# Kernel optimization log

Measured on AMD Instinct MI355X. Metric: run time of the kernel, lower is better.

Reference implementation:

```python
import math
import jax, jax.numpy as jnp
import numpy as np

B, L, D = 8, 2048, 1024
NEG_INF = 1e9  # config.INF stand-in; large finite value keeps fully-masked rows NaN-free


def setup_inputs() -> dict:
    key = jax.random.key(0)
    k1, k2, k3, k4, k5, k6 = jax.random.split(key, 6)
    s = 1.0 / math.sqrt(D)
    return {
        "input_seq": jax.random.normal(k1, (B, L, D), dtype=jnp.float32),
        "input_lens": jax.random.randint(k2, (B,), 1, L + 1, dtype=jnp.int64),
        "output_seq": jax.random.normal(k3, (B, L, D), dtype=jnp.float32),
        "Wk": jax.random.normal(k4, (D, D), dtype=jnp.float32) * s,
        "Wv": jax.random.normal(k5, (D, D), dtype=jnp.float32) * s,
        "Wq": jax.random.normal(k6, (D, D), dtype=jnp.float32) * s,
    }


def reference(input_seq, input_lens, output_seq, Wk, Wv, Wq):
    # Linear(embed_dim, embed_dim, bias=False): y = x @ W^T
    k = jnp.einsum('bld,ed->ble', input_seq, Wk)   # [B, L, D]
    v = jnp.einsum('bld,ed->ble', input_seq, Wv)   # [B, L, D]
    q = jnp.einsum('bld,ed->ble', output_seq, Wq)  # [B, L, D]

    scores = jnp.einsum('bqd,bkd->bqk', q, k) / math.sqrt(D)  # [B, Lq, Lk]

    # Faithful to the torch code (apply_mask=True): mask [B, L] is unsqueezed
    # on the LAST dim -> [B, L, 1], so it broadcasts over the KEY axis and
    # effectively masks query rows with index >= input_lens.
    valid = jnp.arange(L)[None, :] < input_lens[:, None]      # [B, L]
    scores = jnp.where(valid[:, :, None], scores, -NEG_INF)

    attn = jax.nn.softmax(scores, axis=-1)                    # [B, Lq, Lk]
    # dropout is identity in eval mode (deterministic reference)
    context = jnp.einsum('bqk,bkd->bqd', attn, v)             # [B, Lq, D]
    return context, attn
```

## Files before the change

### kernel.cpp

```cpp
#include <hip/hip_runtime.h>
#include <hip/hip_bf16.h>

#define B_ 8
#define L_ 2048
#define D_ 1024
#define CTX_ELEMS (B_ * L_ * D_)

typedef __bf16 bf16x8 __attribute__((ext_vector_type(8)));
typedef float f32x4 __attribute__((ext_vector_type(4)));
typedef unsigned short u16x8 __attribute__((ext_vector_type(8)));
typedef unsigned short u16x4 __attribute__((ext_vector_type(4)));

typedef __attribute__((address_space(1))) void GV;
typedef __attribute__((address_space(3))) void LV;
#define GLL16(g, l) __builtin_amdgcn_global_load_lds((GV*)(g), (LV*)(l), 16, 0, 0)

__device__ __forceinline__ unsigned short f2bf(float f) {
    union { float f; unsigned u; } c; c.f = f;
    unsigned u = c.u;
    u += 0x7fffu + ((u >> 16) & 1u);
    return (unsigned short)(u >> 16);
}

__global__ __launch_bounds__(256) void cvt_kernel(
    const float* __restrict__ x, const float* __restrict__ y,
    const float* __restrict__ Wk, const float* __restrict__ Wv,
    const float* __restrict__ Wq,
    unsigned short* __restrict__ xb, unsigned short* __restrict__ yb,
    unsigned short* __restrict__ wkb, unsigned short* __restrict__ wvb,
    unsigned short* __restrict__ wqb)
{
    const float* src; unsigned short* dst; int n4;
    switch (blockIdx.y) {
        case 0:  src = x;  dst = xb;  n4 = CTX_ELEMS / 4; break;
        case 1:  src = y;  dst = yb;  n4 = CTX_ELEMS / 4; break;
        case 2:  src = Wk; dst = wkb; n4 = D_ * D_ / 4;   break;
        case 3:  src = Wv; dst = wvb; n4 = D_ * D_ / 4;   break;
        default: src = Wq; dst = wqb; n4 = D_ * D_ / 4;   break;
    }
    const int stride = gridDim.x * 256;
    for (int i = blockIdx.x * 256 + threadIdx.x; i < n4; i += stride) {
        float4 f = ((const float4*)src)[i];
        u16x4 o = { f2bf(f.x), f2bf(f.y), f2bf(f.z), f2bf(f.w) };
        ((u16x4*)dst)[i] = o;
    }
}

#define BARx()  __builtin_amdgcn_s_barrier()
#define LGKM0() do { asm volatile("s_waitcnt lgkmcnt(0)" ::: "memory"); \
                     __builtin_amdgcn_sched_barrier(0); } while (0)
#define PRIO(p) __builtin_amdgcn_s_setprio(p)
#define VMW4 asm volatile("s_waitcnt vmcnt(4)" ::: "memory")
#define VMW0 asm volatile("s_waitcnt vmcnt(0)" ::: "memory")

#define G256_VARS \
    const int tid = threadIdx.x; \
    const int wave = tid >> 6, lane = tid & 63; \
    const int wr = wave >> 2, wc = wave & 3; \
    const int lrow = lane & 15, quad = lane >> 4; \
    const int sg_r = lane >> 2; \
    const int sg_c8 = ((lane & 3) ^ ((lane >> 3) & 3)) << 3; \
    const int fsw = (quad ^ ((lrow >> 1) & 3)) << 4; \
    const int pA = (wr * 128 + lrow) * 64 + fsw; \
    const int pB = (wc * 64 + lrow) * 64 + fsw; \
    char* smemc = (char*)smem;

#define STAGE(TT, KH, SRCP, LD, REGOFF) do { \
    const unsigned short* _s = (SRCP) + (size_t)(wave * 32 + sg_r) * (LD) \
                               + (size_t)(TT) * 64 + (KH) * 32 + sg_c8; \
    char* _d = smemc + ((TT) & 1) * 65536 + (REGOFF) + (KH) * 16384 + wave * 2048; \
    GLL16(_s, _d); \
    GLL16(_s + (size_t)16 * (LD), _d + 1024); } while (0)
#define STA(TT, KH) STAGE(TT, KH, Ag2, lda_, 0)
#define STB(TT, KH) STAGE(TT, KH, Bg2, ldb_, 32768)

#define MF16(IOFF, BV) \
    _Pragma("unroll") for (int i = 0; i < 4; i++) \
        _Pragma("unroll") for (int j = 0; j < 4; j++) \
            acc[(IOFF) + i][j] = __builtin_amdgcn_mfma_f32_16x16x32_bf16( \
                av[i], BV[j], acc[(IOFF) + i][j], 0, 0, 0);

#define TILE(T, NT) do { \
    const char* Ab = smemc + ((T) & 1) * 65536; \
    const char* Bb = Ab + 32768; \
    bf16x8 av[4], bv0[4], bv1[4]; \
     \
    _Pragma("unroll") for (int i = 0; i < 4; i++) \
        av[i] = *(const bf16x8*)(Ab + pA + i * 1024); \
    _Pragma("unroll") for (int j = 0; j < 4; j++) \
        bv0[j] = *(const bf16x8*)(Bb + pB + j * 1024); \
    if ((T) + 1 < (NT)) STA((T) + 1, 1); \
    BARx(); LGKM0(); PRIO(1); \
    MF16(0, bv0); \
    PRIO(0); BARx(); \
     \
    _Pragma("unroll") for (int i = 0; i < 4; i++) \
        av[i] = *(const bf16x8*)(Ab + pA + (i + 4) * 1024); \
    if ((T) + 1 < (NT)) STB((T) + 1, 1); \
    BARx(); LGKM0(); PRIO(1); \
    MF16(4, bv0); \
    PRIO(0); BARx(); \
     \
    _Pragma("unroll") for (int i = 0; i < 4; i++) \
        av[i] = *(const bf16x8*)(Ab + 16384 + pA + i * 1024); \
    _Pragma("unroll") for (int j = 0; j < 4; j++) \
        bv1[j] = *(const bf16x8*)(Bb + 16384 + pB + j * 1024); \
    if ((T) + 2 < (NT)) STA((T) + 2, 0); \
    BARx(); LGKM0(); PRIO(1); \
    MF16(0, bv1); \
    PRIO(0); BARx(); \
     \
    _Pragma("unroll") for (int i = 0; i < 4; i++) \
        av[i] = *(const bf16x8*)(Ab + 16384 + pA + (i + 4) * 1024); \
    if ((T) + 2 < (NT)) STB((T) + 2, 0); \
    BARx(); LGKM0(); PRIO(1); \
    MF16(4, bv1); \
    PRIO(0); \
    if ((T) < (NT) - 2)       { VMW4; } \
    else if ((T) == (NT) - 2) { VMW0; } \
    BARx(); \
} while (0)

#define G256_KLOOP(NT) \
    f32x4 acc[8][4]; \
    _Pragma("unroll") for (int i = 0; i < 8; i++) \
        _Pragma("unroll") for (int j = 0; j < 4; j++) \
            acc[i][j] = (f32x4){0.f, 0.f, 0.f, 0.f}; \
    STA(0, 0); STB(0, 0); STA(0, 1); STB(0, 1); STA(1, 0); STB(1, 0); \
    VMW4; BARx(); \
    for (int T = 0; T < (NT); ++T) { TILE(T, (NT)); }

__global__ __launch_bounds__(512, 2) void proj_kernel(
    const unsigned short* __restrict__ xb, const unsigned short* __restrict__ yb,
    const unsigned short* __restrict__ wkb, const unsigned short* __restrict__ wvb,
    const unsigned short* __restrict__ wqb,
    unsigned short* __restrict__ kb, unsigned short* __restrict__ qb,
    unsigned short* __restrict__ vtb)
{
    extern __shared__ unsigned short smem[];
    const int z = blockIdx.z;
    const int lin = blockIdx.x;
    const int xcd = lin & 7, tt = lin >> 3;
    const int big = xcd * 8 + (tt >> 2);
    const int sml = tt & 3;
    int m0, n0;
    const unsigned short *Ag, *Bg;
    if (z == 0)      { Ag = xb;  Bg = wkb; m0 = big * 256; n0 = sml * 256; }
    else if (z == 1) { Ag = wvb; Bg = xb;  m0 = sml * 256; n0 = big * 256; }
    else             { Ag = yb;  Bg = wqb; m0 = big * 256; n0 = sml * 256; }

    G256_VARS
    const int lda_ = D_, ldb_ = D_;
    const unsigned short* Ag2 = Ag + (size_t)m0 * lda_;
    const unsigned short* Bg2 = Bg + (size_t)n0 * ldb_;

    G256_KLOOP(16)

    unsigned short* base; size_t ostride;
    if (z == 1) {
        base = vtb + (size_t)(n0 >> 11) * D_ * L_ + (size_t)m0 * L_ + (n0 & 2047);
        ostride = L_;
    } else {
        base = ((z == 0) ? kb : qb) + (size_t)m0 * D_ + n0;
        ostride = D_;
    }

    __syncthreads();
#pragma unroll
    for (int i = 0; i < 8; i++)
#pragma unroll
        for (int j = 0; j < 4; j++)
#pragma unroll
            for (int r = 0; r < 4; r++) {
                const int row = wr * 128 + i * 16 + quad * 4 + r;
                const int col = wc * 64 + j * 16 + lrow;
                const int off = (row * 512 + col * 2) ^ ((row & 12) << 3);
                *(unsigned short*)((char*)smem + off) = f2bf(acc[i][j][r]);
            }
    __syncthreads();
#pragma unroll
    for (int c = 0; c < 16; c++) {
        const int idx = c * 512 + tid;
        const int rr = idx >> 5, cc = idx & 31;
        const int off = (rr * 512 + cc * 16) ^ ((rr & 12) << 3);
        *(u16x8*)(base + (size_t)rr * ostride + cc * 8)
            = *(const u16x8*)((const char*)smem + off);
    }
}

__global__ __launch_bounds__(512, 2) void scores_kernel(
    const unsigned short* __restrict__ qb, const unsigned short* __restrict__ kb,
    float* __restrict__ attn)
{
    extern __shared__ unsigned short smem[];
    const int bz = blockIdx.z;
    const unsigned short* Ag = qb + (size_t)bz * L_ * D_;
    const unsigned short* Bg = kb + (size_t)bz * L_ * D_;
    float* out = attn + (size_t)bz * L_ * L_;
    const int x = blockIdx.x;
    const int m0 = (x >> 3) * 256, n0 = (x & 7) * 256;

    G256_VARS
    const int lda_ = D_, ldb_ = D_;
    const unsigned short* Ag2 = Ag + (size_t)m0 * lda_;
    const unsigned short* Bg2 = Bg + (size_t)n0 * ldb_;

    G256_KLOOP(16)

#pragma unroll
    for (int i = 0; i < 8; i++) {
        const int m = m0 + wr * 128 + i * 16 + quad * 4;
#pragma unroll
        for (int j = 0; j < 4; j++) {
            const int n = n0 + wc * 64 + j * 16 + lrow;
#pragma unroll
            for (int r = 0; r < 4; r++)
                out[(size_t)(m + r) * L_ + n] = acc[i][j][r] * 0.03125f;
        }
    }
}

__global__ __launch_bounds__(256) void softmax_kernel(
    float* __restrict__ attn, const int* __restrict__ lens,
    unsigned short* __restrict__ attn_bf)
{
    const int r  = blockIdx.x;
    const int b  = r >> 11;
    const int qi = r & 2047;
    float4* rowp = (float4*)(attn + (size_t)r * L_);
    u16x4*  rowb = (u16x4*)(attn_bf + (size_t)r * L_);
    const int tid = threadIdx.x;

    if (qi >= lens[b]) {
        const float u = 1.0f / 2048.0f;
        const unsigned short us = f2bf(u);
        const float4 uf = {u, u, u, u};
        const u16x4 ub = {us, us, us, us};
        rowp[tid] = uf; rowp[tid + 256] = uf;
        rowb[tid] = ub; rowb[tid + 256] = ub;
        return;
    }

    float4 v0 = rowp[tid], v1 = rowp[tid + 256];

    float m = fmaxf(fmaxf(fmaxf(v0.x, v0.y), fmaxf(v0.z, v0.w)),
                    fmaxf(fmaxf(v1.x, v1.y), fmaxf(v1.z, v1.w)));
#pragma unroll
    for (int off = 32; off > 0; off >>= 1) m = fmaxf(m, __shfl_xor(m, off, 64));

    __shared__ float redm[4];
    __shared__ float reds[4];
    const int wave = tid >> 6, lane = tid & 63;
    if (lane == 0) redm[wave] = m;
    __syncthreads();
    m = fmaxf(fmaxf(redm[0], redm[1]), fmaxf(redm[2], redm[3]));

    v0.x = __expf(v0.x - m); v0.y = __expf(v0.y - m);
    v0.z = __expf(v0.z - m); v0.w = __expf(v0.w - m);
    v1.x = __expf(v1.x - m); v1.y = __expf(v1.y - m);
    v1.z = __expf(v1.z - m); v1.w = __expf(v1.w - m);
    float s = (v0.x + v0.y) + (v0.z + v0.w) + (v1.x + v1.y) + (v1.z + v1.w);
#pragma unroll
    for (int off = 32; off > 0; off >>= 1) s += __shfl_xor(s, off, 64);
    if (lane == 0) reds[wave] = s;
    __syncthreads();
    s = reds[0] + reds[1] + reds[2] + reds[3];

    const float inv = 1.0f / s;
    v0.x *= inv; v0.y *= inv; v0.z *= inv; v0.w *= inv;
    v1.x *= inv; v1.y *= inv; v1.z *= inv; v1.w *= inv;
    rowp[tid] = v0; rowp[tid + 256] = v1;
    u16x4 b0 = { f2bf(v0.x), f2bf(v0.y), f2bf(v0.z), f2bf(v0.w) };
    u16x4 b1 = { f2bf(v1.x), f2bf(v1.y), f2bf(v1.z), f2bf(v1.w) };
    rowb[tid] = b0; rowb[tid + 256] = b1;
}

__global__ __launch_bounds__(512, 2) void context_kernel(
    const unsigned short* __restrict__ attn_bf, const unsigned short* __restrict__ vtb,
    float* __restrict__ ctx)
{
    extern __shared__ unsigned short smem[];
    const int bz = blockIdx.z;
    const unsigned short* Ag = attn_bf + (size_t)bz * L_ * L_;
    const unsigned short* Bg = vtb + (size_t)bz * D_ * L_;
    float* out = ctx + (size_t)bz * L_ * D_;
    const int x = blockIdx.x;
    const int m0 = (x & 7) * 256, n0 = (x >> 3) * 256;

    G256_VARS
    const int lda_ = L_, ldb_ = L_;
    const unsigned short* Ag2 = Ag + (size_t)m0 * lda_;
    const unsigned short* Bg2 = Bg + (size_t)n0 * ldb_;

    G256_KLOOP(32)

#pragma unroll
    for (int i = 0; i < 8; i++) {
        const int m = m0 + wr * 128 + i * 16 + quad * 4;
#pragma unroll
        for (int j = 0; j < 4; j++) {
            const int n = n0 + wc * 64 + j * 16 + lrow;
#pragma unroll
            for (int r = 0; r < 4; r++)
                out[(size_t)(m + r) * D_ + n] = acc[i][j][r];
        }
    }
}

extern "C" void kernel_launch(void* const* d_in, const int* in_sizes, int n_in,
                              void* d_out, int out_size, void* d_ws, size_t ws_size,
                              hipStream_t stream) {
    const float* x    = (const float*)d_in[0];
    const int*   lens = (const int*)d_in[1];
    const float* y    = (const float*)d_in[2];
    const float* Wk   = (const float*)d_in[3];
    const float* Wv   = (const float*)d_in[4];
    const float* Wq   = (const float*)d_in[5];

    float* ctx  = (float*)d_out;
    float* attn = (float*)d_out + CTX_ELEMS;

    unsigned short* kb      = (unsigned short*)d_ws;
    unsigned short* qb      = kb + CTX_ELEMS;
    unsigned short* vtb     = qb + CTX_ELEMS;
    unsigned short* attn_bf = (unsigned short*)d_ws;

    unsigned short* xb  = (unsigned short*)attn;
    unsigned short* yb  = xb + CTX_ELEMS;
    unsigned short* wkb = yb + CTX_ELEMS;
    unsigned short* wvb = wkb + D_ * D_;
    unsigned short* wqb = wvb + D_ * D_;

    (void)hipFuncSetAttribute((const void*)proj_kernel,
                              hipFuncAttributeMaxDynamicSharedMemorySize, 131072);
    (void)hipFuncSetAttribute((const void*)scores_kernel,
                              hipFuncAttributeMaxDynamicSharedMemorySize, 131072);
    (void)hipFuncSetAttribute((const void*)context_kernel,
                              hipFuncAttributeMaxDynamicSharedMemorySize, 131072);

    cvt_kernel<<<dim3(2048, 5), 256, 0, stream>>>(x, y, Wk, Wv, Wq,
                                                  xb, yb, wkb, wvb, wqb);
    proj_kernel<<<dim3(256, 1, 3), 512, 131072, stream>>>(xb, yb, wkb, wvb, wqb,
                                                          kb, qb, vtb);
    scores_kernel<<<dim3(64, 1, 8), 512, 131072, stream>>>(qb, kb, attn);
    softmax_kernel<<<dim3(B_ * L_), 256, 0, stream>>>(attn, lens, attn_bf);
    context_kernel<<<dim3(32, 1, 8), 512, 131072, stream>>>(attn_bf, vtb, ctx);
}
```

Before: 569.0 us.

## Use one wave per softmax row, nontemporal stores, and partial LDS waits in GEMM

Softmax now gives each row to a single wavefront, so four rows share a block and the cross-wave LDS reductions and block barriers go away. The fp32 attention and context outputs are written with nontemporal stores to cut cache pollution from large streaming writes. The GEMM tile loop adds an lgkmcnt(4) wait before the barrier, intended to let some LDS reads complete earlier. Each wave now holds 32 floats per lane, which raises register use, and the changes touch several kernels at once.

Result: no change. 567.0 us (-0.4%).

```diff
diff --git a/kernel.cpp b/kernel.cpp
--- a/kernel.cpp
+++ b/kernel.cpp
@@ -49,6 +49,7 @@
 #define BARx()  __builtin_amdgcn_s_barrier()
 #define LGKM0() do { asm volatile("s_waitcnt lgkmcnt(0)" ::: "memory"); \
                      __builtin_amdgcn_sched_barrier(0); } while (0)
+#define LGKM4() asm volatile("s_waitcnt lgkmcnt(4)" ::: "memory")
 #define PRIO(p) __builtin_amdgcn_s_setprio(p)
 #define VMW4 asm volatile("s_waitcnt vmcnt(4)" ::: "memory")
 #define VMW0 asm volatile("s_waitcnt vmcnt(0)" ::: "memory")
@@ -90,7 +91,7 @@
     _Pragma("unroll") for (int j = 0; j < 4; j++) \
         bv0[j] = *(const bf16x8*)(Bb + pB + j * 1024); \
     if ((T) + 1 < (NT)) STA((T) + 1, 1); \
-    BARx(); LGKM0(); PRIO(1); \
+    LGKM4(); BARx(); LGKM0(); PRIO(1); \
     MF16(0, bv0); \
     PRIO(0); BARx(); \
      \
@@ -106,7 +107,7 @@
     _Pragma("unroll") for (int j = 0; j < 4; j++) \
         bv1[j] = *(const bf16x8*)(Bb + 16384 + pB + j * 1024); \
     if ((T) + 2 < (NT)) STA((T) + 2, 0); \
-    BARx(); LGKM0(); PRIO(1); \
+    LGKM4(); BARx(); LGKM0(); PRIO(1); \
     MF16(0, bv1); \
     PRIO(0); BARx(); \
      \
@@ -224,55 +225,55 @@
     float* __restrict__ attn, const int* __restrict__ lens,
     unsigned short* __restrict__ attn_bf)
 {
-    const int r  = blockIdx.x;
+    const int wave = threadIdx.x >> 6, lane = threadIdx.x & 63;
+    const int r  = blockIdx.x * 4 + wave;
     const int b  = r >> 11;
     const int qi = r & 2047;
-    float4* rowp = (float4*)(attn + (size_t)r * L_);
-    u16x4*  rowb = (u16x4*)(attn_bf + (size_t)r * L_);
-    const int tid = threadIdx.x;
+    f32x4* rowp = (f32x4*)(attn + (size_t)r * L_);
+    u16x4* rowb = (u16x4*)(attn_bf + (size_t)r * L_);
 
     if (qi >= lens[b]) {
         const float u = 1.0f / 2048.0f;
         const unsigned short us = f2bf(u);
-        const float4 uf = {u, u, u, u};
+        const f32x4 uf = {u, u, u, u};
         const u16x4 ub = {us, us, us, us};
-        rowp[tid] = uf; rowp[tid + 256] = uf;
-        rowb[tid] = ub; rowb[tid + 256] = ub;
+#pragma unroll
+        for (int c = 0; c < 8; c++) {
+            __builtin_nontemporal_store(uf, &rowp[lane + 64 * c]);
+            rowb[lane + 64 * c] = ub;
+        }
         return;
     }
 
-    float4 v0 = rowp[tid], v1 = rowp[tid + 256];
-
-    float m = fmaxf(fmaxf(fmaxf(v0.x, v0.y), fmaxf(v0.z, v0.w)),
-                    fmaxf(fmaxf(v1.x, v1.y), fmaxf(v1.z, v1.w)));
+    f32x4 v[8];
+#pragma unroll
+    for (int c = 0; c < 8; c++) v[c] = rowp[lane + 64 * c];
+
+    float m = -1e30f;
+#pragma unroll
+    for (int c = 0; c < 8; c++)
+        m = fmaxf(m, fmaxf(fmaxf(v[c][0], v[c][1]), fmaxf(v[c][2], v[c][3])));
 #pragma unroll
     for (int off = 32; off > 0; off >>= 1) m = fmaxf(m, __shfl_xor(m, off, 64));
 
-    __shared__ float redm[4];
-    __shared__ float reds[4];
-    const int wave = tid >> 6, lane = tid & 63;
-    if (lane == 0) redm[wave] = m;
-    __syncthreads();
-    m = fmaxf(fmaxf(redm[0], redm[1]), fmaxf(redm[2], redm[3]));
-
-    v0.x = __expf(v0.x - m); v0.y = __expf(v0.y - m);
-    v0.z = __expf(v0.z - m); v0.w = __expf(v0.w - m);
-    v1.x = __expf(v1.x - m); v1.y = __expf(v1.y - m);
-    v1.z = __expf(v1.z - m); v1.w = __expf(v1.w - m);
-    float s = (v0.x + v0.y) + (v0.z + v0.w) + (v1.x + v1.y) + (v1.z + v1.w);
+    float s = 0.f;
+#pragma unroll
+    for (int c = 0; c < 8; c++) {
+        v[c][0] = __expf(v[c][0] - m); v[c][1] = __expf(v[c][1] - m);
+        v[c][2] = __expf(v[c][2] - m); v[c][3] = __expf(v[c][3] - m);
+        s += (v[c][0] + v[c][1]) + (v[c][2] + v[c][3]);
+    }
 #pragma unroll
     for (int off = 32; off > 0; off >>= 1) s += __shfl_xor(s, off, 64);
-    if (lane == 0) reds[wave] = s;
-    __syncthreads();
-    s = reds[0] + reds[1] + reds[2] + reds[3];
 
     const float inv = 1.0f / s;
-    v0.x *= inv; v0.y *= inv; v0.z *= inv; v0.w *= inv;
-    v1.x *= inv; v1.y *= inv; v1.z *= inv; v1.w *= inv;
-    rowp[tid] = v0; rowp[tid + 256] = v1;
-    u16x4 b0 = { f2bf(v0.x), f2bf(v0.y), f2bf(v0.z), f2bf(v0.w) };
-    u16x4 b1 = { f2bf(v1.x), f2bf(v1.y), f2bf(v1.z), f2bf(v1.w) };
-    rowb[tid] = b0; rowb[tid + 256] = b1;
+#pragma unroll
+    for (int c = 0; c < 8; c++) {
+        v[c][0] *= inv; v[c][1] *= inv; v[c][2] *= inv; v[c][3] *= inv;
+        __builtin_nontemporal_store(v[c], &rowp[lane + 64 * c]);
+        u16x4 bb = { f2bf(v[c][0]), f2bf(v[c][1]), f2bf(v[c][2]), f2bf(v[c][3]) };
+        rowb[lane + 64 * c] = bb;
+    }
 }
 
 __global__ __launch_bounds__(512, 2) void context_kernel(
@@ -302,7 +303,8 @@
             const int n = n0 + wc * 64 + j * 16 + lrow;
 #pragma unroll
             for (int r = 0; r < 4; r++)
-                out[(size_t)(m + r) * D_ + n] = acc[i][j][r];
+                __builtin_nontemporal_store(acc[i][j][r],
+                    &out[(size_t)(m + r) * D_ + n]);
         }
     }
 }
@@ -343,6 +345,6 @@
     proj_kernel<<<dim3(256, 1, 3), 512, 131072, stream>>>(xb, yb, wkb, wvb, wqb,
                                                           kb, qb, vtb);
     scores_kernel<<<dim3(64, 1, 8), 512, 131072, stream>>>(qb, kb, attn);
-    softmax_kernel<<<dim3(B_ * L_), 256, 0, stream>>>(attn, lens, attn_bf);
+    softmax_kernel<<<dim3(B_ * L_ / 4), 256, 0, stream>>>(attn, lens, attn_bf);
     context_kernel<<<dim3(32, 1, 8), 512, 131072, stream>>>(attn_bf, vtb, ctx);
 }
```
